# Performance work log

Hardware: AMD Instinct MI355X
Metric: run time of the kernel (lower is better)

## Reference

```python
import jax, jax.numpy as jnp
import numpy as np

N_HEADS = 16

def setup_inputs() -> dict:
    key = jax.random.key(0)
    ks = jax.random.split(key, 8)
    bs, t, h, dh = 32, 512, 1024, 64
    s = lambda k, shape: jax.random.normal(k, shape, dtype=jnp.float32) * 0.02
    return {
        "x": jax.random.normal(ks[0], (bs, t, h), dtype=jnp.float32),
        "Wq": s(ks[1], (h, h)),
        "bq": s(ks[2], (h,)),
        "Wk": s(ks[3], (h, h)),
        "bk": s(ks[4], (h,)),
        "Wv": s(ks[5], (h, dh)),
        "bv": s(ks[6], (dh,)),
        "Wo": s(ks[7], (dh, h)),
    }

def reference(x, Wq, bq, Wk, bk, Wv, bv, Wo):
    bs, t, h = x.shape
    dh = Wv.shape[1]
    nh = N_HEADS
    # projections (context == x; static_features=None path)
    q = (x @ Wq + bq).reshape(bs, t, nh, dh)   # [b,t,h,d]
    k = (x @ Wk + bk).reshape(bs, t, nh, dh)
    v = x @ Wv + bv                             # shared single-head V: [b,t,d]
    scale = dh ** -0.5
    # per-head scores [b,h,q,k]
    score = jnp.einsum('bqhd,bkhd->bhqk', q, k) * scale
    # causal mask (mask_future_timesteps=True): -inf above diagonal
    mask = jnp.triu(jnp.full((t, t), -jnp.inf, dtype=score.dtype), 1)
    score = score + mask
    prob = jax.nn.softmax(score, axis=-1)       # attn_dropout is identity (p=0)
    # broadcast shared V across heads
    attn_vec = jnp.einsum('bhqk,bkd->bhqd', prob, v)   # [b,h,t,d]
    m_attn_vec = jnp.mean(attn_vec, axis=1)            # head-mean pooling [b,t,d]
    out = m_attn_vec @ Wo                              # out_proj, no bias; out_dropout identity
    return out, attn_vec
```

## Files before the change

kernel.cpp:

```cpp
#include <hip/hip_runtime.h>
#include <hip/hip_bf16.h>
#include <math.h>

#define BS 32
#define TT 512
#define HH 1024
#define NH 16
#define DH 64
#define MM (BS*TT)
#define NCAT 2176

typedef __attribute__((ext_vector_type(8))) __bf16 bf16x8;
typedef __attribute__((ext_vector_type(4))) float  f32x4;

#define QSCALE 0.18033688011112042f

#if __has_builtin(__builtin_amdgcn_exp2f)
#define EXP2F(x) __builtin_amdgcn_exp2f(x)
#else
#define EXP2F(x) __expf((x) * 0.69314718055994531f)
#endif

__device__ __forceinline__ void gld16(const void* g, void* l) {
    __builtin_amdgcn_global_load_lds(
        (const __attribute__((address_space(1))) unsigned int*)g,
        (__attribute__((address_space(3))) unsigned int*)l,
        16, 0, 0);
}

__global__ __launch_bounds__(256) void cvt_x(const float* __restrict__ x,
                                             __bf16* __restrict__ xb)
{
    const size_t i = ((size_t)blockIdx.x * 256 + threadIdx.x) * 8;
    float4 a = *(const float4*)(x + i);
    float4 b = *(const float4*)(x + i + 4);
    bf16x8 v;
    v[0] = (__bf16)a.x; v[1] = (__bf16)a.y; v[2] = (__bf16)a.z; v[3] = (__bf16)a.w;
    v[4] = (__bf16)b.x; v[5] = (__bf16)b.y; v[6] = (__bf16)b.z; v[7] = (__bf16)b.w;
    *(bf16x8*)(xb + i) = v;
}

__global__ __launch_bounds__(256) void prep_w(
    const float* __restrict__ Wq, const float* __restrict__ Wk,
    const float* __restrict__ Wv, const float* __restrict__ bq_,
    const float* __restrict__ bk_, const float* __restrict__ bv_,
    __bf16* __restrict__ Wt, float* __restrict__ bias_cat)
{
    __shared__ __align__(16) __bf16 tile[64][72];
    const int tid = threadIdx.x;
    const int n0 = blockIdx.x * 64;
    const int k0 = blockIdx.y * 64;

    const int n_l = tid & 63;
    const int k_b = tid >> 6;
    const int n   = n0 + n_l;
    #pragma unroll
    for (int j = 0; j < 16; ++j) {
        const int k_l = j * 4 + k_b;
        const int k   = k0 + k_l;
        float v;
        if (n < 1024)      v = Wq[(size_t)k * 1024 + n];
        else if (n < 2048) v = Wk[(size_t)k * 1024 + (n - 1024)];
        else if (n < 2112) v = Wv[(size_t)k * 64 + (n - 2048)];
        else               v = 0.f;
        tile[n_l][k_l] = (__bf16)v;
    }
    if (blockIdx.y == 0 && tid < 64) {
        const int nn = n0 + tid;
        bias_cat[nn] = (nn < 1024) ? bq_[nn]
                     : (nn < 2048) ? bk_[nn - 1024]
                     : (nn < 2112) ? bv_[nn - 2048] : 0.f;
    }
    __syncthreads();
    const int n_l2 = tid >> 2;
    const int k_l2 = (tid & 3) * 16;
    __bf16* dst = Wt + (size_t)(n0 + n_l2) * 1024 + k0 + k_l2;
    *(bf16x8*)dst       = *(const bf16x8*)&tile[n_l2][k_l2];
    *(bf16x8*)(dst + 8) = *(const bf16x8*)&tile[n_l2][k_l2 + 8];
}

__global__ __launch_bounds__(256) void gemm_qkv(
    const __bf16* __restrict__ A, const __bf16* __restrict__ B,
    const float* __restrict__ bias_cat,
    __bf16* __restrict__ Qo, __bf16* __restrict__ Ko,
    __bf16* __restrict__ Vt)
{
    __shared__ __align__(16) __bf16 sA[128 * 32];
    __shared__ __align__(16) __bf16 sB[128 * 32];

    const int tid  = threadIdx.x;
    const int wv   = tid >> 6;
    const int ln   = tid & 63;
    const int quad = ln >> 4;
    const int l16  = ln & 15;

    const int orig = blockIdx.y * 17 + blockIdx.x;
    const int swz  = (orig & 7) * 272 + (orig >> 3);
    const int m0 = (swz / 17) * 128;
    const int n0 = (swz % 17) * 128;

    const int rw = (wv & 1) * 64;
    const int cw = (wv >> 1) * 64;

    f32x4 acc[4][4];
    #pragma unroll
    for (int i = 0; i < 4; ++i)
        #pragma unroll
        for (int j = 0; j < 4; ++j) acc[i][j] = f32x4{0, 0, 0, 0};

    const int srow = wv * 16 + (ln >> 2);
    const int scol = (ln & 3) * 8;
    const __bf16* ga0 = A + (size_t)(m0 + srow) * 1024 + scol;
    const __bf16* gb0 = B + (size_t)(n0 + srow) * 1024 + scol;
    __bf16* la0 = sA + wv * 512;
    __bf16* lb0 = sB + wv * 512;

    for (int k0 = 0; k0 < 1024; k0 += 32) {
        gld16(ga0 + k0, la0);
        gld16(ga0 + (size_t)64 * 1024 + k0, la0 + 2048);
        gld16(gb0 + k0, lb0);
        gld16(gb0 + (size_t)64 * 1024 + k0, lb0 + 2048);
        __syncthreads();

        bf16x8 af[4], bfr[4];
        #pragma unroll
        for (int mt = 0; mt < 4; ++mt)
            af[mt] = *(const bf16x8*)&sA[(rw + mt * 16 + l16) * 32 + quad * 8];
        #pragma unroll
        for (int nt = 0; nt < 4; ++nt)
            bfr[nt] = *(const bf16x8*)&sB[(cw + nt * 16 + l16) * 32 + quad * 8];
        #pragma unroll
        for (int mt = 0; mt < 4; ++mt)
            #pragma unroll
            for (int nt = 0; nt < 4; ++nt)
                acc[mt][nt] = __builtin_amdgcn_mfma_f32_16x16x32_bf16(af[mt], bfr[nt], acc[mt][nt], 0, 0, 0);
        __syncthreads();
    }

    #pragma unroll
    for (int mt = 0; mt < 4; ++mt) {
        #pragma unroll
        for (int nt = 0; nt < 4; ++nt) {
            const int colb = n0 + cw + nt * 16 + l16;
            if (colb >= 2112) continue;
            const float bias = bias_cat[colb];
            #pragma unroll
            for (int r = 0; r < 4; ++r) {
                const int row = m0 + rw + mt * 16 + quad * 4 + r;
                const int b = row >> 9, t = row & 511;
                float v = acc[mt][nt][r] + bias;
                if (colb < 1024) {
                    const int h = colb >> 6, d = colb & 63;
                    Qo[(((size_t)(b * NH + h) * TT) + t) * DH + d] = (__bf16)(v * QSCALE);
                } else if (colb < 2048) {
                    const int c = colb - 1024;
                    const int h = c >> 6, d = c & 63;
                    Ko[(((size_t)(b * NH + h) * TT) + t) * DH + d] = (__bf16)v;
                } else {
                    const int d = colb - 2048;
                    Vt[((size_t)(b * DH + d)) * TT + t] = (__bf16)v;
                }
            }
        }
    }
}

__global__ __launch_bounds__(1024) void attn_mfma(
    const __bf16* __restrict__ Q, const __bf16* __restrict__ K,
    const __bf16* __restrict__ Vt, float* __restrict__ attn_vec,
    float* __restrict__ mav)
{
    __shared__ __align__(16) __bf16 sV[64][512];
    __shared__ float smav[32][65];

    const int bid  = blockIdx.x;
    const int qt2  = (bid < 256) ? (15 - (bid >> 5)) : ((bid - 256) >> 5);
    const int b    = bid & 31;
    const int wave = threadIdx.x >> 6;
    const int lane = threadIdx.x & 63;
    const int quad = lane >> 4;
    const int l16  = lane & 15;
    const int bh   = b * NH + wave;
    const int q0   = qt2 << 5;
    const int kend = q0 + 32;

    {
        float* p = &smav[0][0];
        p[threadIdx.x] = 0.f;
        p[threadIdx.x + 1024] = 0.f;
        if (threadIdx.x < 32) p[threadIdx.x + 2048] = 0.f;
    }

    const __bf16* Vb = Vt + (size_t)b * DH * TT;
    const int svw = wave & 7;
    #pragma unroll
    for (int r = 0; r < 4; ++r) {
        const int row = wave + r * 16;
        gld16(Vb + (size_t)row * TT + ((lane ^ svw) * 8), &sV[row][0]);
    }

    const __bf16* Qbh = Q + (size_t)bh * TT * DH;
    const __bf16* Kbh = K + (size_t)bh * TT * DH;

    const int perm = ((l16 >> 2) << 3) + (l16 & 3);
    const __bf16* kp1 = Kbh + (size_t)perm * DH;
    const __bf16* kp2 = Kbh + (size_t)(perm + 4) * DH;

    const bf16x8 qA_lo = *(const bf16x8*)(Qbh + (size_t)(q0 + l16) * DH + quad * 8);
    const bf16x8 qA_hi = *(const bf16x8*)(Qbh + (size_t)(q0 + l16) * DH + 32 + quad * 8);
    const bf16x8 qB_lo = *(const bf16x8*)(Qbh + (size_t)(q0 + 16 + l16) * DH + quad * 8);
    const bf16x8 qB_hi = *(const bf16x8*)(Qbh + (size_t)(q0 + 16 + l16) * DH + 32 + quad * 8);

    f32x4 OA[4] = {f32x4{0,0,0,0}, f32x4{0,0,0,0}, f32x4{0,0,0,0}, f32x4{0,0,0,0}};
    f32x4 OB[4] = {f32x4{0,0,0,0}, f32x4{0,0,0,0}, f32x4{0,0,0,0}, f32x4{0,0,0,0}};
    float lA = 0.f, lB = 0.f;

    bf16x8 c1a = *(const bf16x8*)(kp1 + quad * 8);
    bf16x8 c1b = *(const bf16x8*)(kp1 + 32 + quad * 8);
    bf16x8 c2a = *(const bf16x8*)(kp2 + quad * 8);
    bf16x8 c2b = *(const bf16x8*)(kp2 + 32 + quad * 8);
    const int kb1 = (32 < kend) ? 32 : 0;
    bf16x8 n1a = *(const bf16x8*)(kp1 + (size_t)kb1 * DH + quad * 8);
    bf16x8 n1b = *(const bf16x8*)(kp1 + (size_t)kb1 * DH + 32 + quad * 8);
    bf16x8 n2a = *(const bf16x8*)(kp2 + (size_t)kb1 * DH + quad * 8);
    bf16x8 n2b = *(const bf16x8*)(kp2 + (size_t)kb1 * DH + 32 + quad * 8);

    const int sx = l16 & 7;

    __syncthreads();

    for (int kb0 = 0; kb0 < kend; kb0 += 32) {
        const int vg = (((kb0 >> 3) + quad) ^ sx) * 8;
        bf16x8 vf0 = *(const bf16x8*)&sV[l16][vg];
        bf16x8 vf1 = *(const bf16x8*)&sV[16 + l16][vg];
        bf16x8 vf2 = *(const bf16x8*)&sV[32 + l16][vg];
        bf16x8 vf3 = *(const bf16x8*)&sV[48 + l16][vg];

        __builtin_amdgcn_s_setprio(1);
        f32x4 s1A = __builtin_amdgcn_mfma_f32_16x16x32_bf16(c1a, qA_lo, f32x4{0,0,0,0}, 0, 0, 0);
        s1A       = __builtin_amdgcn_mfma_f32_16x16x32_bf16(c1b, qA_hi, s1A, 0, 0, 0);
        f32x4 s2A = __builtin_amdgcn_mfma_f32_16x16x32_bf16(c2a, qA_lo, f32x4{0,0,0,0}, 0, 0, 0);
        s2A       = __builtin_amdgcn_mfma_f32_16x16x32_bf16(c2b, qA_hi, s2A, 0, 0, 0);
        f32x4 s1B = __builtin_amdgcn_mfma_f32_16x16x32_bf16(c1a, qB_lo, f32x4{0,0,0,0}, 0, 0, 0);
        s1B       = __builtin_amdgcn_mfma_f32_16x16x32_bf16(c1b, qB_hi, s1B, 0, 0, 0);
        f32x4 s2B = __builtin_amdgcn_mfma_f32_16x16x32_bf16(c2a, qB_lo, f32x4{0,0,0,0}, 0, 0, 0);
        s2B       = __builtin_amdgcn_mfma_f32_16x16x32_bf16(c2b, qB_hi, s2B, 0, 0, 0);
        __builtin_amdgcn_s_setprio(0);

        if (kb0 == q0) {
            const int qqA = q0 + l16, qqB = q0 + 16 + l16;
            #pragma unroll
            for (int r = 0; r < 4; ++r) {
                const int key1 = kb0 + quad * 8 + r;
                const int key2 = key1 + 4;
                if (key1 > qqA) s1A[r] = -INFINITY;
                if (key2 > qqA) s2A[r] = -INFINITY;
                if (key1 > qqB) s1B[r] = -INFINITY;
                if (key2 > qqB) s2B[r] = -INFINITY;
            }
        }

        bf16x8 pfA, pfB;
        float psA0 = 0.f, psA1 = 0.f, psB0 = 0.f, psB1 = 0.f;
        #pragma unroll
        for (int r = 0; r < 4; ++r) {
            float pa0 = EXP2F(s1A[r]);
            float pa1 = EXP2F(s2A[r]);
            float pb0 = EXP2F(s1B[r]);
            float pb1 = EXP2F(s2B[r]);
            psA0 += pa0; psA1 += pa1;
            psB0 += pb0; psB1 += pb1;
            pfA[r]     = (__bf16)pa0;
            pfA[4 + r] = (__bf16)pa1;
            pfB[r]     = (__bf16)pb0;
            pfB[4 + r] = (__bf16)pb1;
        }
        lA += psA0 + psA1;
        lB += psB0 + psB1;

        __builtin_amdgcn_s_setprio(1);
        OA[0] = __builtin_amdgcn_mfma_f32_16x16x32_bf16(pfA, vf0, OA[0], 0, 0, 0);
        OB[0] = __builtin_amdgcn_mfma_f32_16x16x32_bf16(pfB, vf0, OB[0], 0, 0, 0);
        OA[1] = __builtin_amdgcn_mfma_f32_16x16x32_bf16(pfA, vf1, OA[1], 0, 0, 0);
        OB[1] = __builtin_amdgcn_mfma_f32_16x16x32_bf16(pfB, vf1, OB[1], 0, 0, 0);
        OA[2] = __builtin_amdgcn_mfma_f32_16x16x32_bf16(pfA, vf2, OA[2], 0, 0, 0);
        OB[2] = __builtin_amdgcn_mfma_f32_16x16x32_bf16(pfB, vf2, OB[2], 0, 0, 0);
        OA[3] = __builtin_amdgcn_mfma_f32_16x16x32_bf16(pfA, vf3, OA[3], 0, 0, 0);
        OB[3] = __builtin_amdgcn_mfma_f32_16x16x32_bf16(pfB, vf3, OB[3], 0, 0, 0);
        __builtin_amdgcn_s_setprio(0);

        c1a = n1a; c1b = n1b; c2a = n2a; c2b = n2b;
        const int kbn = (kb0 + 64 < kend) ? kb0 + 64 : kend - 32;
        const __bf16* nk1 = kp1 + (size_t)kbn * DH;
        const __bf16* nk2 = kp2 + (size_t)kbn * DH;
        n1a = *(const bf16x8*)(nk1 + quad * 8);
        n1b = *(const bf16x8*)(nk1 + 32 + quad * 8);
        n2a = *(const bf16x8*)(nk2 + quad * 8);
        n2b = *(const bf16x8*)(nk2 + 32 + quad * 8);
    }

    lA += __shfl_xor(lA, 16);
    lA += __shfl_xor(lA, 32);
    lB += __shfl_xor(lB, 16);
    lB += __shfl_xor(lB, 32);

    #pragma unroll
    for (int r = 0; r < 4; ++r) {
        const float invA = 1.0f / __shfl(lA, quad * 4 + r);
        const float invB = 1.0f / __shfl(lB, quad * 4 + r);
        const int ltA = quad * 4 + r;
        const int ltB = ltA + 16;
        const int tA = q0 + ltA;
        const int tB = q0 + ltB;
        float* opA = attn_vec + ((size_t)bh * TT + tA) * DH + l16;
        float* opB = attn_vec + ((size_t)bh * TT + tB) * DH + l16;
        #pragma unroll
        for (int nt = 0; nt < 4; ++nt) {
            const float vA = OA[nt][r] * invA;
            const float vB = OB[nt][r] * invB;
            opA[nt * 16] = vA;
            opB[nt * 16] = vB;
            atomicAdd(&smav[ltA][nt * 16 + l16], vA * (1.f / 16.f));
            atomicAdd(&smav[ltB][nt * 16 + l16], vB * (1.f / 16.f));
        }
    }

    __syncthreads();

    if (threadIdx.x < 512) {
        const int row = threadIdx.x >> 4;
        const int d0  = (threadIdx.x & 15) * 4;
        float4 v;
        v.x = smav[row][d0];
        v.y = smav[row][d0 + 1];
        v.z = smav[row][d0 + 2];
        v.w = smav[row][d0 + 3];
        *(float4*)(mav + ((size_t)(b * TT + q0 + row)) * DH + d0) = v;
    }
}

__global__ __launch_bounds__(256) void gemm_out(
    const float* __restrict__ A, const float* __restrict__ B,
    float* __restrict__ C, int M, int N, int K)
{
    __shared__ __align__(16) __bf16 sA[64][32];
    __shared__ __align__(16) __bf16 sB[64][32];

    const int tid  = threadIdx.x;
    const int wave = tid >> 6;
    const int lane = tid & 63;
    const int m0 = blockIdx.y * 64;
    const int n0 = blockIdx.x * 64;

    f32x4 acc[4] = {f32x4{0,0,0,0}, f32x4{0,0,0,0}, f32x4{0,0,0,0}, f32x4{0,0,0,0}};

    const int ar = tid >> 2;
    const int ac = (tid & 3) * 8;
    const int bk = tid >> 3;
    const int bc = (tid & 7) * 8;
    const int quad = lane >> 4;
    const int l16  = lane & 15;

    for (int k0 = 0; k0 < K; k0 += 32) {
        const float* ap = A + (size_t)(m0 + ar) * K + k0 + ac;
        float4 a0 = *(const float4*)ap;
        float4 a1 = *(const float4*)(ap + 4);
        {
            bf16x8 av;
            av[0] = (__bf16)a0.x; av[1] = (__bf16)a0.y; av[2] = (__bf16)a0.z; av[3] = (__bf16)a0.w;
            av[4] = (__bf16)a1.x; av[5] = (__bf16)a1.y; av[6] = (__bf16)a1.z; av[7] = (__bf16)a1.w;
            *(bf16x8*)&sA[ar][ac] = av;
        }
        const float* bp = B + (size_t)(k0 + bk) * N + n0 + bc;
        float4 b0 = *(const float4*)bp;
        float4 b1 = *(const float4*)(bp + 4);
        sB[bc + 0][bk] = (__bf16)b0.x;
        sB[bc + 1][bk] = (__bf16)b0.y;
        sB[bc + 2][bk] = (__bf16)b0.z;
        sB[bc + 3][bk] = (__bf16)b0.w;
        sB[bc + 4][bk] = (__bf16)b1.x;
        sB[bc + 5][bk] = (__bf16)b1.y;
        sB[bc + 6][bk] = (__bf16)b1.z;
        sB[bc + 7][bk] = (__bf16)b1.w;
        __syncthreads();

        bf16x8 afrag = *(const bf16x8*)&sA[wave * 16 + l16][quad * 8];
        #pragma unroll
        for (int tn = 0; tn < 4; ++tn) {
            bf16x8 bfrag = *(const bf16x8*)&sB[tn * 16 + l16][quad * 8];
            acc[tn] = __builtin_amdgcn_mfma_f32_16x16x32_bf16(afrag, bfrag, acc[tn], 0, 0, 0);
        }
        __syncthreads();
    }

    #pragma unroll
    for (int tn = 0; tn < 4; ++tn) {
        #pragma unroll
        for (int r = 0; r < 4; ++r) {
            int row = m0 + wave * 16 + quad * 4 + r;
            int col = n0 + tn * 16 + l16;
            C[(size_t)row * N + col] = acc[tn][r];
        }
    }
}

extern "C" void kernel_launch(void* const* d_in, const int* in_sizes, int n_in,
                              void* d_out, int out_size, void* d_ws, size_t ws_size,
                              hipStream_t stream)
{
    const float* x  = (const float*)d_in[0];
    const float* Wq = (const float*)d_in[1];
    const float* bq = (const float*)d_in[2];
    const float* Wk = (const float*)d_in[3];
    const float* bk = (const float*)d_in[4];
    const float* Wv = (const float*)d_in[5];
    const float* bv = (const float*)d_in[6];
    const float* Wo = (const float*)d_in[7];

    float* out      = (float*)d_out;
    float* attn_vec = out + (size_t)MM * HH;

    char* ws = (char*)d_ws;
    __bf16* xb  = (__bf16*)ws;
    __bf16* Wt  = xb + (size_t)MM * HH;
    float* bias_cat = (float*)(Wt + (size_t)NCAT * HH);
    __bf16* Qb  = (__bf16*)(bias_cat + 2304);
    __bf16* Kb  = Qb + (size_t)MM * HH;
    __bf16* Vt  = Kb + (size_t)MM * HH;
    float*  mav = (float*)xb;

    cvt_x<<<MM * HH / (256 * 8), 256, 0, stream>>>(x, xb);
    prep_w<<<dim3(NCAT / 64, HH / 64), 256, 0, stream>>>(Wq, Wk, Wv, bq, bk, bv, Wt, bias_cat);
    gemm_qkv<<<dim3(NCAT / 128, MM / 128), 256, 0, stream>>>(xb, Wt, bias_cat, Qb, Kb, Vt);
    attn_mfma<<<BS * NH, 1024, 0, stream>>>(Qb, Kb, Vt, attn_vec, mav);
    gemm_out<<<dim3(HH / 64, MM / 64), 256, 0, stream>>>(mav, Wo, out, MM, HH, DH);
}
```

Before: 439.2 us.

## Map attention blocks per (batch, head) with K staged in LDS, separate head-mean reduction

Each attention block now handles one (batch, head) pair, with its 16 waves covering different query tiles in a balanced pairing. The block stages that head's full K into swizzled shared memory once, so K fragments come from LDS instead of per-wave prefetched global loads. The head-mean pooling moves out of the kernel, dropping the shared-memory atomics, into a separate reduce_heads kernel that re-reads attn_vec from global memory. The setprio hints are also removed. The cost is an extra 64KB of LDS per block, an extra launch and an extra pass over attn_vec.

```diff
diff --git a/kernel.cpp b/kernel.cpp
--- a/kernel.cpp
+++ b/kernel.cpp
@@ -167,76 +167,75 @@
 
 __global__ __launch_bounds__(1024) void attn_mfma(
     const __bf16* __restrict__ Q, const __bf16* __restrict__ K,
-    const __bf16* __restrict__ Vt, float* __restrict__ attn_vec,
-    float* __restrict__ mav)
-{
+    const __bf16* __restrict__ Vt, float* __restrict__ attn_vec)
+{
+    __shared__ __align__(16) __bf16 sK[512 * 64];
     __shared__ __align__(16) __bf16 sV[64][512];
-    __shared__ float smav[32][65];
-
-    const int bid  = blockIdx.x;
-    const int qt2  = (bid < 256) ? (15 - (bid >> 5)) : ((bid - 256) >> 5);
-    const int b    = bid & 31;
+
+    const int bh   = blockIdx.x;
+    const int b    = bh >> 4;
     const int wave = threadIdx.x >> 6;
     const int lane = threadIdx.x & 63;
     const int quad = lane >> 4;
     const int l16  = lane & 15;
-    const int bh   = b * NH + wave;
+
+    const int s_ = wave & 3, j_ = wave >> 2;
+    const int qt2 = (j_ == 0) ? s_ : (j_ == 1) ? (7 - s_) : (j_ == 2) ? (8 + s_) : (15 - s_);
     const int q0   = qt2 << 5;
     const int kend = q0 + 32;
 
-    {
-        float* p = &smav[0][0];
-        p[threadIdx.x] = 0.f;
-        p[threadIdx.x + 1024] = 0.f;
-        if (threadIdx.x < 32) p[threadIdx.x + 2048] = 0.f;
-    }
-
-    const __bf16* Vb = Vt + (size_t)b * DH * TT;
+    const __bf16* Qbh = Q + (size_t)bh * TT * DH;
+    const __bf16* Kbh = K + (size_t)bh * TT * DH;
+    const __bf16* Vb  = Vt + (size_t)b * DH * TT;
+
+    #pragma unroll
+    for (int r = 0; r < 4; ++r) {
+        const int c   = wave * 4 + r;
+        const int row = c * 8 + (lane >> 3);
+        const int p   = lane & 7;
+        const int swz = (row & 3) | (((row >> 3) & 1) << 2);
+        gld16(Kbh + (size_t)row * DH + ((p ^ swz) * 8), sK + (size_t)c * 512);
+    }
     const int svw = wave & 7;
     #pragma unroll
     for (int r = 0; r < 4; ++r) {
         const int row = wave + r * 16;
         gld16(Vb + (size_t)row * TT + ((lane ^ svw) * 8), &sV[row][0]);
     }
-
-    const __bf16* Qbh = Q + (size_t)bh * TT * DH;
-    const __bf16* Kbh = K + (size_t)bh * TT * DH;
-
-    const int perm = ((l16 >> 2) << 3) + (l16 & 3);
-    const __bf16* kp1 = Kbh + (size_t)perm * DH;
-    const __bf16* kp2 = Kbh + (size_t)(perm + 4) * DH;
 
     const bf16x8 qA_lo = *(const bf16x8*)(Qbh + (size_t)(q0 + l16) * DH + quad * 8);
     const bf16x8 qA_hi = *(const bf16x8*)(Qbh + (size_t)(q0 + l16) * DH + 32 + quad * 8);
     const bf16x8 qB_lo = *(const bf16x8*)(Qbh + (size_t)(q0 + 16 + l16) * DH + quad * 8);
     const bf16x8 qB_hi = *(const bf16x8*)(Qbh + (size_t)(q0 + 16 + l16) * DH + 32 + quad * 8);
 
+    const int perm = ((l16 >> 2) << 3) + (l16 & 3);
+    const int swzl = (l16 & 3) | (((l16 >> 2) & 1) << 2);
+    const __bf16* k1lo = sK + (size_t)perm * DH       + (( quad      ^ swzl) * 8);
+    const __bf16* k1hi = sK + (size_t)perm * DH       + (((quad | 4) ^ swzl) * 8);
+    const __bf16* k2lo = sK + (size_t)(perm + 4) * DH + (( quad      ^ swzl) * 8);
+    const __bf16* k2hi = sK + (size_t)(perm + 4) * DH + (((quad | 4) ^ swzl) * 8);
+
+    const int sx = l16 & 7;
+
     f32x4 OA[4] = {f32x4{0,0,0,0}, f32x4{0,0,0,0}, f32x4{0,0,0,0}, f32x4{0,0,0,0}};
     f32x4 OB[4] = {f32x4{0,0,0,0}, f32x4{0,0,0,0}, f32x4{0,0,0,0}, f32x4{0,0,0,0}};
     float lA = 0.f, lB = 0.f;
 
-    bf16x8 c1a = *(const bf16x8*)(kp1 + quad * 8);
-    bf16x8 c1b = *(const bf16x8*)(kp1 + 32 + quad * 8);
-    bf16x8 c2a = *(const bf16x8*)(kp2 + quad * 8);
-    bf16x8 c2b = *(const bf16x8*)(kp2 + 32 + quad * 8);
-    const int kb1 = (32 < kend) ? 32 : 0;
-    bf16x8 n1a = *(const bf16x8*)(kp1 + (size_t)kb1 * DH + quad * 8);
-    bf16x8 n1b = *(const bf16x8*)(kp1 + (size_t)kb1 * DH + 32 + quad * 8);
-    bf16x8 n2a = *(const bf16x8*)(kp2 + (size_t)kb1 * DH + quad * 8);
-    bf16x8 n2b = *(const bf16x8*)(kp2 + (size_t)kb1 * DH + 32 + quad * 8);
-
-    const int sx = l16 & 7;
-
     __syncthreads();
 
     for (int kb0 = 0; kb0 < kend; kb0 += 32) {
+        const int ko = kb0 * DH;
+        bf16x8 c1a = *(const bf16x8*)(k1lo + ko);
+        bf16x8 c1b = *(const bf16x8*)(k1hi + ko);
+        bf16x8 c2a = *(const bf16x8*)(k2lo + ko);
+        bf16x8 c2b = *(const bf16x8*)(k2hi + ko);
+
         const int vg = (((kb0 >> 3) + quad) ^ sx) * 8;
         bf16x8 vf0 = *(const bf16x8*)&sV[l16][vg];
         bf16x8 vf1 = *(const bf16x8*)&sV[16 + l16][vg];
         bf16x8 vf2 = *(const bf16x8*)&sV[32 + l16][vg];
         bf16x8 vf3 = *(const bf16x8*)&sV[48 + l16][vg];
 
-        __builtin_amdgcn_s_setprio(1);
         f32x4 s1A = __builtin_amdgcn_mfma_f32_16x16x32_bf16(c1a, qA_lo, f32x4{0,0,0,0}, 0, 0, 0);
         s1A       = __builtin_amdgcn_mfma_f32_16x16x32_bf16(c1b, qA_hi, s1A, 0, 0, 0);
         f32x4 s2A = __builtin_amdgcn_mfma_f32_16x16x32_bf16(c2a, qA_lo, f32x4{0,0,0,0}, 0, 0, 0);
@@ -245,7 +244,6 @@
         s1B       = __builtin_amdgcn_mfma_f32_16x16x32_bf16(c1b, qB_hi, s1B, 0, 0, 0);
         f32x4 s2B = __builtin_amdgcn_mfma_f32_16x16x32_bf16(c2a, qB_lo, f32x4{0,0,0,0}, 0, 0, 0);
         s2B       = __builtin_amdgcn_mfma_f32_16x16x32_bf16(c2b, qB_hi, s2B, 0, 0, 0);
-        __builtin_amdgcn_s_setprio(0);
 
         if (kb0 == q0) {
             const int qqA = q0 + l16, qqB = q0 + 16 + l16;
@@ -278,7 +276,6 @@
         lA += psA0 + psA1;
         lB += psB0 + psB1;
 
-        __builtin_amdgcn_s_setprio(1);
         OA[0] = __builtin_amdgcn_mfma_f32_16x16x32_bf16(pfA, vf0, OA[0], 0, 0, 0);
         OB[0] = __builtin_amdgcn_mfma_f32_16x16x32_bf16(pfB, vf0, OB[0], 0, 0, 0);
         OA[1] = __builtin_amdgcn_mfma_f32_16x16x32_bf16(pfA, vf1, OA[1], 0, 0, 0);
@@ -287,16 +284,6 @@
         OB[2] = __builtin_amdgcn_mfma_f32_16x16x32_bf16(pfB, vf2, OB[2], 0, 0, 0);
         OA[3] = __builtin_amdgcn_mfma_f32_16x16x32_bf16(pfA, vf3, OA[3], 0, 0, 0);
         OB[3] = __builtin_amdgcn_mfma_f32_16x16x32_bf16(pfB, vf3, OB[3], 0, 0, 0);
-        __builtin_amdgcn_s_setprio(0);
-
-        c1a = n1a; c1b = n1b; c2a = n2a; c2b = n2b;
-        const int kbn = (kb0 + 64 < kend) ? kb0 + 64 : kend - 32;
-        const __bf16* nk1 = kp1 + (size_t)kbn * DH;
-        const __bf16* nk2 = kp2 + (size_t)kbn * DH;
-        n1a = *(const bf16x8*)(nk1 + quad * 8);
-        n1b = *(const bf16x8*)(nk1 + 32 + quad * 8);
-        n2a = *(const bf16x8*)(nk2 + quad * 8);
-        n2b = *(const bf16x8*)(nk2 + 32 + quad * 8);
     }
 
     lA += __shfl_xor(lA, 16);
@@ -308,35 +295,37 @@
     for (int r = 0; r < 4; ++r) {
         const float invA = 1.0f / __shfl(lA, quad * 4 + r);
         const float invB = 1.0f / __shfl(lB, quad * 4 + r);
-        const int ltA = quad * 4 + r;
-        const int ltB = ltA + 16;
-        const int tA = q0 + ltA;
-        const int tB = q0 + ltB;
+        const int tA = q0 + quad * 4 + r;
+        const int tB = tA + 16;
         float* opA = attn_vec + ((size_t)bh * TT + tA) * DH + l16;
         float* opB = attn_vec + ((size_t)bh * TT + tB) * DH + l16;
         #pragma unroll
         for (int nt = 0; nt < 4; ++nt) {
-            const float vA = OA[nt][r] * invA;
-            const float vB = OB[nt][r] * invB;
-            opA[nt * 16] = vA;
-            opB[nt * 16] = vB;
-            atomicAdd(&smav[ltA][nt * 16 + l16], vA * (1.f / 16.f));
-            atomicAdd(&smav[ltB][nt * 16 + l16], vB * (1.f / 16.f));
-        }
-    }
-
-    __syncthreads();
-
-    if (threadIdx.x < 512) {
-        const int row = threadIdx.x >> 4;
-        const int d0  = (threadIdx.x & 15) * 4;
-        float4 v;
-        v.x = smav[row][d0];
-        v.y = smav[row][d0 + 1];
-        v.z = smav[row][d0 + 2];
-        v.w = smav[row][d0 + 3];
-        *(float4*)(mav + ((size_t)(b * TT + q0 + row)) * DH + d0) = v;
-    }
+            opA[nt * 16] = OA[nt][r] * invA;
+            opB[nt * 16] = OB[nt][r] * invB;
+        }
+    }
+}
+
+__global__ __launch_bounds__(256) void reduce_heads(
+    const float* __restrict__ av, float* __restrict__ mav)
+{
+    const size_t idx = (size_t)blockIdx.x * 256 + threadIdx.x;
+    const int    d4  = (int)(idx & 15);
+    const size_t bt  = idx >> 4;
+    const int    b   = (int)(bt >> 9);
+    const int    t   = (int)(bt & 511);
+    const float4* p = (const float4*)av + (((size_t)b * NH * TT) + t) * 16 + d4;
+    float4 a = p[0];
+    #pragma unroll
+    for (int h = 1; h < NH; ++h) {
+        float4 v = p[(size_t)h * TT * 16];
+        a.x += v.x; a.y += v.y; a.z += v.z; a.w += v.w;
+    }
+    float4 o;
+    o.x = a.x * (1.f / 16.f); o.y = a.y * (1.f / 16.f);
+    o.z = a.z * (1.f / 16.f); o.w = a.w * (1.f / 16.f);
+    ((float4*)mav)[idx] = o;
 }
 
 __global__ __launch_bounds__(256) void gemm_out(
@@ -432,6 +421,7 @@
     cvt_x<<<MM * HH / (256 * 8), 256, 0, stream>>>(x, xb);
     prep_w<<<dim3(NCAT / 64, HH / 64), 256, 0, stream>>>(Wq, Wk, Wv, bq, bk, bv, Wt, bias_cat);
     gemm_qkv<<<dim3(NCAT / 128, MM / 128), 256, 0, stream>>>(xb, Wt, bias_cat, Qb, Kb, Vt);
-    attn_mfma<<<BS * NH, 1024, 0, stream>>>(Qb, Kb, Vt, attn_vec, mav);
+    attn_mfma<<<BS * NH, 1024, 0, stream>>>(Qb, Kb, Vt, attn_vec);
+    reduce_heads<<<(MM * DH / 4) / 256, 256, 0, stream>>>(attn_vec, mav);
     gemm_out<<<dim3(HH / 64, MM / 64), 256, 0, stream>>>(mav, Wo, out, MM, HH, DH);
 }
```

New measurement: 359.2 us. -18.2%, faster.
